# Performance work log

Measured on AMD Instinct MI355X. Metric: run time of the kernel, lower is better.

The kernel has to match this reference:

```python
import jax
jax.config.update("jax_enable_x64", True)
import jax.numpy as jnp
import numpy as np

B = 1_000_000

def _generators():
    # 8 sl(3) basis elements, each scaled by its (unit) weight, float64.
    e = np.zeros((8, 3, 3), dtype=np.float64)
    e[0, 0, 2] = 1.0                      # x translation
    e[1, 1, 2] = 1.0                      # y translation
    e[2, 0, 1] = -1.0; e[2, 1, 0] = 1.0   # rotation
    e[3, 0, 0] = 1.0; e[3, 1, 1] = 1.0; e[3, 2, 2] = -2.0  # scale
    e[4, 0, 0] = 1.0; e[4, 1, 1] = -1.0   # stretch
    e[5, 0, 1] = 1.0; e[5, 1, 0] = 1.0    # shear
    e[6, 2, 0] = 1.0                      # x keystone
    e[7, 2, 1] = 1.0                      # y keystone
    weights = np.ones((8,), dtype=np.float64)  # all weight kwargs default to 1.0
    return jnp.asarray(e * weights[:, None, None])

_GEN = _generators()

def setup_inputs() -> dict:
    key = jax.random.key(0)
    lie_vectors = jax.random.normal(key, (B, 8), dtype=jnp.float32)
    return {"lie_vectors": lie_vectors}

def reference(lie_vectors) -> jnp.ndarray:
    # Weighted sum of generators in float64: (B,8) x (8,3,3) -> (B,3,3)
    A = jnp.einsum("bk,kij->bij", lie_vectors.astype(jnp.float64), _GEN)
    # Batched matrix exponential of tiny 3x3 matrices
    H = jax.vmap(jax.scipy.linalg.expm)(A)
    # Homogeneous normalization by the (2,2) entry
    H = H / H[:, 2:3, 2:3]
    return H.astype(jnp.float32)
```

## Files before the change

### kernel.cpp

```cpp
#include <hip/hip_runtime.h>
#include <math.h>

__device__ __forceinline__ void mm3(const double* __restrict__ A,
                                    const double* __restrict__ Bm,
                                    double* __restrict__ C) {
#pragma unroll
    for (int i = 0; i < 3; ++i) {
#pragma unroll
        for (int j = 0; j < 3; ++j) {
            C[i*3+j] = fma(A[i*3+0], Bm[0*3+j],
                       fma(A[i*3+1], Bm[1*3+j],
                           A[i*3+2] * Bm[2*3+j]));
        }
    }
}

__global__ __launch_bounds__(256) void lie_expm_kernel(const float* __restrict__ v,
                                                       float* __restrict__ out,
                                                       int n) {
    int tid = blockIdx.x * blockDim.x + threadIdx.x;
    if (tid >= n) return;

    const float4* vv = reinterpret_cast<const float4*>(v);
    float4 p0 = vv[2*(size_t)tid + 0];
    float4 p1 = vv[2*(size_t)tid + 1];
    double x0 = p0.x, x1 = p0.y, x2 = p0.z, x3 = p0.w;
    double x4 = p1.x, x5 = p1.y, x6 = p1.z, x7 = p1.w;

    double A[9];
    A[0] = x3 + x4;  A[1] = x5 - x2;  A[2] = x0;
    A[3] = x2 + x5;  A[4] = x3 - x4;  A[5] = x1;
    A[6] = x6;       A[7] = x7;       A[8] = -2.0 * x3;

    double c0 = fabs(A[0]) + fabs(A[3]) + fabs(A[6]);
    double c1 = fabs(A[1]) + fabs(A[4]) + fabs(A[7]);
    double c2 = fabs(A[2]) + fabs(A[5]) + fabs(A[8]);
    double nrm = fmax(c0, fmax(c1, c2));

    int s = 0;
    while (nrm > 0.25) { nrm *= 0.5; ++s; }
    double sc = ldexp(1.0, -s);
#pragma unroll
    for (int i = 0; i < 9; ++i) A[i] *= sc;

    double E[9], P[9], T[9];
#pragma unroll
    for (int i = 0; i < 9; ++i) { E[i] = A[i]; P[i] = A[i]; }
    E[0] += 1.0; E[4] += 1.0; E[8] += 1.0;

    const double rn[13] = {1.0/2, 1.0/3, 1.0/4, 1.0/5, 1.0/6, 1.0/7, 1.0/8,
                           1.0/9, 1.0/10, 1.0/11, 1.0/12, 1.0/13, 1.0/14};
#pragma unroll
    for (int k = 0; k < 13; ++k) {
        mm3(P, A, T);
#pragma unroll
        for (int i = 0; i < 9; ++i) { P[i] = T[i] * rn[k]; E[i] += P[i]; }
    }

    for (int i = 0; i < s; ++i) {
        mm3(E, E, T);
#pragma unroll
        for (int j = 0; j < 9; ++j) E[j] = T[j];
    }

    double inv = 1.0 / E[8];
    float* o = out + (size_t)tid * 9;
#pragma unroll
    for (int i = 0; i < 9; ++i) o[i] = (float)(E[i] * inv);
}

extern "C" void kernel_launch(void* const* d_in, const int* in_sizes, int n_in,
                              void* d_out, int out_size, void* d_ws, size_t ws_size,
                              hipStream_t stream) {
    const float* v = (const float*)d_in[0];
    float* out = (float*)d_out;
    int n = in_sizes[0] / 8;
    int block = 256;
    int grid = (n + block - 1) / block;
    lie_expm_kernel<<<grid, block, 0, stream>>>(v, out, n);
}
```

Before: 100.9 us.

## Use Padé-13 scaling-and-squaring expm and coalesce output stores via LDS

Replaces the 13-term Taylor series with theta-0.25 scaling by the Higham Padé(13) approximant, which uses a larger theta so fewer squarings are needed. It computes A2/A4/A6, builds U and V, and solves via an explicit 3x3 inverse. Output is staged through shared memory so global writes are contiguous instead of 9-float strided per thread. The approach needs fewer fp64 matrix multiplies and squarings at the cost of a division, extra registers and more LDS.

```diff
diff --git a/kernel.cpp b/kernel.cpp
--- a/kernel.cpp
+++ b/kernel.cpp
@@ -15,58 +15,129 @@
     }
 }
 
-__global__ __launch_bounds__(256) void lie_expm_kernel(const float* __restrict__ v,
-                                                       float* __restrict__ out,
-                                                       int n) {
-    int tid = blockIdx.x * blockDim.x + threadIdx.x;
-    if (tid >= n) return;
+#define BLOCK 256
 
-    const float4* vv = reinterpret_cast<const float4*>(v);
-    float4 p0 = vv[2*(size_t)tid + 0];
-    float4 p1 = vv[2*(size_t)tid + 1];
-    double x0 = p0.x, x1 = p0.y, x2 = p0.z, x3 = p0.w;
-    double x4 = p1.x, x5 = p1.y, x6 = p1.z, x7 = p1.w;
+__global__ __launch_bounds__(BLOCK) void lie_expm_kernel(const float* __restrict__ v,
+                                                         float* __restrict__ out,
+                                                         int n) {
+    __shared__ float lds[BLOCK * 9];
 
-    double A[9];
-    A[0] = x3 + x4;  A[1] = x5 - x2;  A[2] = x0;
-    A[3] = x2 + x5;  A[4] = x3 - x4;  A[5] = x1;
-    A[6] = x6;       A[7] = x7;       A[8] = -2.0 * x3;
+    int tid = threadIdx.x;
+    int gid = blockIdx.x * BLOCK + tid;
+    bool active = gid < n;
 
-    double c0 = fabs(A[0]) + fabs(A[3]) + fabs(A[6]);
-    double c1 = fabs(A[1]) + fabs(A[4]) + fabs(A[7]);
-    double c2 = fabs(A[2]) + fabs(A[5]) + fabs(A[8]);
-    double nrm = fmax(c0, fmax(c1, c2));
+    float oloc[9];
 
-    int s = 0;
-    while (nrm > 0.25) { nrm *= 0.5; ++s; }
-    double sc = ldexp(1.0, -s);
+    if (active) {
+        const float4* vv = reinterpret_cast<const float4*>(v);
+        float4 p0 = vv[2*(size_t)gid + 0];
+        float4 p1 = vv[2*(size_t)gid + 1];
+        double x0 = p0.x, x1 = p0.y, x2 = p0.z, x3 = p0.w;
+        double x4 = p1.x, x5 = p1.y, x6 = p1.z, x7 = p1.w;
+
+        double A[9];
+        A[0] = x3 + x4;  A[1] = x5 - x2;  A[2] = x0;
+        A[3] = x2 + x5;  A[4] = x3 - x4;  A[5] = x1;
+        A[6] = x6;       A[7] = x7;       A[8] = -2.0 * x3;
+
+        double c0 = fabs(A[0]) + fabs(A[3]) + fabs(A[6]);
+        double c1 = fabs(A[1]) + fabs(A[4]) + fabs(A[7]);
+        double c2 = fabs(A[2]) + fabs(A[5]) + fabs(A[8]);
+        double nrm = fmax(c0, fmax(c1, c2));
+
+        const double theta13 = 5.371920351148152;
+        double r = nrm * (1.0 / theta13);
+        int s = 0;
+        if (r > 1.0) {
+            int hi = __double2hiint(r);
+            s = ((hi >> 20) & 0x7ff) - 1023 + 1;
+        }
+        double sc = __hiloint2double((1023 - s) << 20, 0);
 #pragma unroll
-    for (int i = 0; i < 9; ++i) A[i] *= sc;
+        for (int i = 0; i < 9; ++i) A[i] *= sc;
 
-    double E[9], P[9], T[9];
+        const double b0  = 64764752532480000.0, b1  = 32382376266240000.0;
+        const double b2  = 7771770303897600.0,  b3  = 1187353796428800.0;
+        const double b4  = 129060195264000.0,   b5  = 10559470521600.0;
+        const double b6  = 670442572800.0,      b7  = 33522128640.0;
+        const double b8  = 1323241920.0,        b9  = 40840800.0;
+        const double b10 = 960960.0,            b11 = 16380.0;
+        const double b12 = 182.0,               b13 = 1.0;
+
+        double A2[9], A4[9], A6[9];
+        mm3(A, A, A2);
+        mm3(A2, A2, A4);
+        mm3(A4, A2, A6);
+
+        double W[9], V[9];
 #pragma unroll
-    for (int i = 0; i < 9; ++i) { E[i] = A[i]; P[i] = A[i]; }
-    E[0] += 1.0; E[4] += 1.0; E[8] += 1.0;
+        for (int i = 0; i < 9; ++i)
+            W[i] = fma(b12, A6[i], fma(b10, A4[i], b8 * A2[i]));
+        mm3(A6, W, V);
+#pragma unroll
+        for (int i = 0; i < 9; ++i)
+            V[i] += fma(b6, A6[i], fma(b4, A4[i], b2 * A2[i]));
+        V[0] += b0; V[4] += b0; V[8] += b0;
 
-    const double rn[13] = {1.0/2, 1.0/3, 1.0/4, 1.0/5, 1.0/6, 1.0/7, 1.0/8,
-                           1.0/9, 1.0/10, 1.0/11, 1.0/12, 1.0/13, 1.0/14};
+        double Z[9], U[9];
 #pragma unroll
-    for (int k = 0; k < 13; ++k) {
-        mm3(P, A, T);
+        for (int i = 0; i < 9; ++i)
+            W[i] = fma(b13, A6[i], fma(b11, A4[i], b9 * A2[i]));
+        mm3(A6, W, Z);
 #pragma unroll
-        for (int i = 0; i < 9; ++i) { P[i] = T[i] * rn[k]; E[i] += P[i]; }
+        for (int i = 0; i < 9; ++i)
+            Z[i] += fma(b7, A6[i], fma(b5, A4[i], b3 * A2[i]));
+        Z[0] += b1; Z[4] += b1; Z[8] += b1;
+        mm3(A, Z, U);
+
+        double M[9], R[9];
+#pragma unroll
+        for (int i = 0; i < 9; ++i) { M[i] = V[i] - U[i]; R[i] = V[i] + U[i]; }
+
+        double inv[9];
+        inv[0] = fma(M[4], M[8], -M[5]*M[7]);
+        inv[1] = fma(M[2], M[7], -M[1]*M[8]);
+        inv[2] = fma(M[1], M[5], -M[2]*M[4]);
+        inv[3] = fma(M[5], M[6], -M[3]*M[8]);
+        inv[4] = fma(M[0], M[8], -M[2]*M[6]);
+        inv[5] = fma(M[2], M[3], -M[0]*M[5]);
+        inv[6] = fma(M[3], M[7], -M[4]*M[6]);
+        inv[7] = fma(M[1], M[6], -M[0]*M[7]);
+        inv[8] = fma(M[0], M[4], -M[1]*M[3]);
+        double det = fma(M[0], inv[0], fma(M[1], inv[3], M[2]*inv[6]));
+        double rd = 1.0 / det;
+#pragma unroll
+        for (int i = 0; i < 9; ++i) inv[i] *= rd;
+
+        double E[9], T[9];
+        mm3(inv, R, E);
+
+        for (int i = 0; i < s; ++i) {
+            mm3(E, E, T);
+#pragma unroll
+            for (int j = 0; j < 9; ++j) E[j] = T[j];
+        }
+
+        double invh = 1.0 / E[8];
+#pragma unroll
+        for (int i = 0; i < 9; ++i) oloc[i] = (float)(E[i] * invh);
     }
 
-    for (int i = 0; i < s; ++i) {
-        mm3(E, E, T);
+    if (active) {
 #pragma unroll
-        for (int j = 0; j < 9; ++j) E[j] = T[j];
+        for (int j = 0; j < 9; ++j) lds[tid * 9 + j] = oloc[j];
     }
+    __syncthreads();
 
-    double inv = 1.0 / E[8];
-    float* o = out + (size_t)tid * 9;
+    size_t base = (size_t)blockIdx.x * (BLOCK * 9);
+    int count = n - blockIdx.x * BLOCK;
+    if (count > BLOCK) count = BLOCK;
+    int total = count * 9;
 #pragma unroll
-    for (int i = 0; i < 9; ++i) o[i] = (float)(E[i] * inv);
+    for (int i = 0; i < 9; ++i) {
+        int idx = i * BLOCK + tid;
+        if (idx < total) out[base + idx] = lds[idx];
+    }
 }
 
 extern "C" void kernel_launch(void* const* d_in, const int* in_sizes, int n_in,
@@ -75,7 +146,6 @@
     const float* v = (const float*)d_in[0];
     float* out = (float*)d_out;
     int n = in_sizes[0] / 8;
-    int block = 256;
-    int grid = (n + block - 1) / block;
-    lie_expm_kernel<<<grid, block, 0, stream>>>(v, out, n);
+    int grid = (n + BLOCK - 1) / BLOCK;
+    lie_expm_kernel<<<grid, BLOCK, 0, stream>>>(v, out, n);
 }
```

Result: faster. 89.42 us (-11.3%).
